# Kernel tuning notes

Hardware: AMD Instinct MI355X
Metric: run time of the kernel (lower is better)

Reference implementation:

```python
import jax, jax.numpy as jnp
import numpy as np

N, E, D_IN, D_OUT = 100000, 1600000, 64, 64


def setup_inputs() -> dict:
    key = jax.random.key(0)
    k0, k1, k2, k3 = jax.random.split(key, 4)
    x = jax.random.normal(k0, (N, D_IN), dtype=jnp.float32)
    edge_index = jax.random.randint(k1, (2, E), 0, N)  # [2, E] (src, dst)
    W = jax.random.normal(k2, (D_IN, D_OUT), dtype=jnp.float32) / np.sqrt(D_IN).astype(np.float32)
    b = jnp.zeros((D_OUT,), dtype=jnp.float32)
    causal_attention = jax.random.normal(k3, (D_OUT, D_OUT), dtype=jnp.float32)
    return {"x": x, "edge_index": edge_index, "W": W, "b": b,
            "causal_attention": causal_attention, "L": 1}


def gcn_conv(x, edge_index, W, b):
    # PyG GCNConv: x' = D^{-1/2} (A + I) D^{-1/2} (x W) + b
    n = x.shape[0]
    xw = x @ W  # [N, D_OUT]
    loops = jnp.arange(n)
    src = jnp.concatenate([edge_index[0], loops])  # [E+N]
    dst = jnp.concatenate([edge_index[1], loops])
    deg = jax.ops.segment_sum(jnp.ones_like(src, dtype=xw.dtype), dst, num_segments=n)
    dinv = jnp.where(deg > 0, jax.lax.rsqrt(deg), 0.0)
    norm = dinv[src] * dinv[dst]  # [E+N]
    agg = jax.ops.segment_sum(norm[:, None] * xw[src], dst, num_segments=n)  # [N, D_OUT]
    return agg + b


def reference(x, edge_index, W, b, causal_attention, L):
    x_conv = gcn_conv(x, edge_index, W, b)
    causal_weights = jax.nn.softmax(causal_attention, axis=1)  # row softmax
    return x_conv @ causal_weights  # [N, D_OUT]
```

## Files before the change

kernel.cpp:

```cpp
#include <hip/hip_runtime.h>
#include <hip/hip_bf16.h>


#define D 64
#define BSHIFT 7
#define BNODES 128
#define ARENA_CAP 3072
#define BIN_TILE 8192

__device__ __forceinline__ unsigned short f2bf(float f) {
    union { float f; unsigned int u; } c;
    c.f = f;
    unsigned int u = c.u;
    u += 0x7fffu + ((u >> 16) & 1u);
    return (unsigned short)(u >> 16);
}
__device__ __forceinline__ float bflo(unsigned int u) {
    union { unsigned int u; float f; } c;
    c.u = u << 16;
    return c.f;
}
__device__ __forceinline__ float bfhi(unsigned int u) {
    union { unsigned int u; float f; } c;
    c.u = u & 0xffff0000u;
    return c.f;
}

__global__ __launch_bounds__(256) void prep_kernel(const float* __restrict__ W,
                                                   const float* __restrict__ b,
                                                   const float* __restrict__ A,
                                                   float* __restrict__ M,
                                                   float* __restrict__ bs,
                                                   int* __restrict__ cursor, int nbuck) {
    __shared__ float S[D * D];
    int t = threadIdx.x;
    int gidx = blockIdx.x * 256 + t;
    if (gidx < nbuck) cursor[gidx] = gidx * ARENA_CAP;
    int wv = t >> 6, lane = t & 63;
#pragma unroll 4
    for (int rr = 0; rr < 16; rr++) {
        int r = wv * 16 + rr;
        float a = A[r * D + lane];
        float m = a;
        for (int off = 32; off; off >>= 1) m = fmaxf(m, __shfl_xor(m, off));
        float p = __expf(a - m);
        float ssum = p;
        for (int off = 32; off; off >>= 1) ssum += __shfl_xor(ssum, off);
        S[r * D + lane] = p / ssum;
    }
    __syncthreads();
    int k = blockIdx.x * 4 + wv;
    float acc = 0.f;
    for (int d2 = 0; d2 < D; d2++) acc += W[k * D + d2] * S[d2 * D + lane];
    M[k * D + lane] = acc;
    if (blockIdx.x == 0 && t < D) {
        float a2 = 0.f;
        for (int d2 = 0; d2 < D; d2++) a2 += b[d2] * S[d2 * D + t];
        bs[t] = a2;
    }
}

__global__ __launch_bounds__(512) void bin_kernel(const int* __restrict__ src,
                                                  const int* __restrict__ dst,
                                                  int* __restrict__ cursor,
                                                  int* __restrict__ binned, int E) {
    __shared__ int h[1024];
    int t = threadIdx.x;
    for (int i = t; i < 1024; i += 512) h[i] = 0;
    __syncthreads();
    int base = blockIdx.x * BIN_TILE;
    int pv[16], bk[16], rv[16];
#pragma unroll
    for (int k = 0; k < 16; k++) {
        int e = base + k * 512 + t;
        if (e < E) {
            int s = src[e], d = dst[e];
            bk[k] = (d >> BSHIFT) & 1023;
            pv[k] = (s << BSHIFT) | (d & (BNODES - 1));
            rv[k] = atomicAdd(&h[bk[k]], 1);
        }
    }
    __syncthreads();
    for (int b2 = t; b2 < 1024; b2 += 512) {
        int c = h[b2];
        if (c) h[b2] = atomicAdd(&cursor[b2], c);
    }
    __syncthreads();
#pragma unroll
    for (int k = 0; k < 16; k++) {
        int e = base + k * 512 + t;
        if (e < E) binned[h[bk[k]] + rv[k]] = pv[k];
    }
}

__global__ __launch_bounds__(256) void rebin_zmat_kernel(const float* __restrict__ x,
                                                         const float* __restrict__ M,
                                                         int* __restrict__ binned,
                                                         const int* __restrict__ cursor,
                                                         int* __restrict__ rowstart,
                                                         int* __restrict__ rowend,
                                                         float* __restrict__ dinv,
                                                         unsigned short* __restrict__ zbf,
                                                         int N) {
    __shared__ int buf[ARENA_CAP];
    __shared__ float Ms[D * D];
    __shared__ float xs[16][D + 1];
    __shared__ float dv[BNODES];
    __shared__ int h[BNODES];
    __shared__ int sc[BNODES];
    __shared__ int cur[BNODES];
    int t = threadIdx.x;
    int b = blockIdx.x;
    int s = b * ARENA_CAP;
    int cnt = cursor[b] - s;
    if (cnt > ARENA_CAP) cnt = ARENA_CAP;
    for (int i = t; i < (D * D) / 4; i += 256)
        ((float4*)Ms)[i] = ((const float4*)M)[i];
    if (t < BNODES) h[t] = 0;
    __syncthreads();
    for (int i = t; i < cnt; i += 256) {
        int p = binned[s + i];
        buf[i] = p;
        atomicAdd(&h[p & (BNODES - 1)], 1);
    }
    __syncthreads();
    if (t < BNODES) sc[t] = h[t];
    __syncthreads();
    for (int off = 1; off < BNODES; off <<= 1) {
        int u = (t < BNODES && t >= off) ? sc[t - off] : 0;
        __syncthreads();
        if (t < BNODES) sc[t] += u;
        __syncthreads();
    }
    if (t < BNODES) {
        int ex = sc[t] - h[t];
        cur[t] = ex;
        float di = rsqrtf((float)(h[t] + 1));
        dv[t] = di;
        int node = (b << BSHIFT) + t;
        if (node < N) {
            rowstart[node] = s + ex;
            rowend[node] = s + sc[t];
            dinv[node] = di;
        }
    }
    __syncthreads();
    for (int i = t; i < cnt; i += 256) {
        int p = buf[i];
        int pos = atomicAdd(&cur[p & (BNODES - 1)], 1);
        binned[s + pos] = (int)((unsigned)p >> BSHIFT);
    }
    for (int rc = 0; rc < 8; rc++) {
        __syncthreads();
        int row0 = (b << BSHIFT) + rc * 16;
        for (int i = t; i < 16 * D; i += 256) {
            int r = i >> 6, c = i & 63;
            xs[r][c] = (row0 + r < N) ? x[(size_t)(row0 + r) * D + c] : 0.f;
        }
        __syncthreads();
        int r = t >> 4;
        int jg = (t & 15) << 2;
        float4 acc = {0.f, 0.f, 0.f, 0.f};
#pragma unroll
        for (int k = 0; k < D; k++) {
            float xv = xs[r][k];
            float4 m = *(const float4*)&Ms[k * D + jg];
            acc.x += xv * m.x;
            acc.y += xv * m.y;
            acc.z += xv * m.z;
            acc.w += xv * m.w;
        }
        int row = row0 + r;
        if (row < N) {
            float di = dv[rc * 16 + r];
            ushort4 res;
            res.x = f2bf(di * acc.x);
            res.y = f2bf(di * acc.y);
            res.z = f2bf(di * acc.z);
            res.w = f2bf(di * acc.w);
            *(ushort4*)&zbf[(size_t)row * D + jg] = res;
        }
    }
}

__global__ __launch_bounds__(256) void gather_kernel(const unsigned short* __restrict__ zbf,
                                                     const int* __restrict__ csr,
                                                     const int* __restrict__ rowstart,
                                                     const int* __restrict__ rowend,
                                                     const float* __restrict__ dinv,
                                                     const float* __restrict__ bs,
                                                     float* __restrict__ out, int n) {
    int node = blockIdx.x * 4 + (threadIdx.x >> 6);
    if (node >= n) return;
    int lane = threadIdx.x & 63;
    int g = lane >> 5;
    int c = lane & 31;
    int start = rowstart[node];
    int end = rowend[node];
    float a0 = 0.f, a1 = 0.f, a2 = 0.f, a3 = 0.f;
    int e = start;
    while (e < end) {
        int cnt = min(end - e, 64);
        int sreg = (lane < cnt) ? csr[e + lane] : 0;
        int k = 0;
        for (; k + 7 < cnt; k += 8) {
            int p0 = __shfl(sreg, k + g);
            int p1 = __shfl(sreg, k + 2 + g);
            int p2 = __shfl(sreg, k + 4 + g);
            int p3 = __shfl(sreg, k + 6 + g);
            unsigned u0 = *(const unsigned*)&zbf[(size_t)p0 * D + 2 * c];
            unsigned u1 = *(const unsigned*)&zbf[(size_t)p1 * D + 2 * c];
            unsigned u2 = *(const unsigned*)&zbf[(size_t)p2 * D + 2 * c];
            unsigned u3 = *(const unsigned*)&zbf[(size_t)p3 * D + 2 * c];
            a0 += bflo(u0); a1 += bfhi(u0);
            a2 += bflo(u1); a3 += bfhi(u1);
            a0 += bflo(u2); a1 += bfhi(u2);
            a2 += bflo(u3); a3 += bfhi(u3);
        }
        for (; k + 1 < cnt; k += 2) {
            int p = __shfl(sreg, k + g);
            unsigned u = *(const unsigned*)&zbf[(size_t)p * D + 2 * c];
            a0 += bflo(u); a1 += bfhi(u);
        }
        if (k < cnt) {
            int p = __shfl(sreg, k);
            unsigned u = *(const unsigned*)&zbf[(size_t)p * D + 2 * c];
            if (g == 0) { a0 += bflo(u); a1 += bfhi(u); }
        }
        e += cnt;
    }
    a0 += a2; a1 += a3;
    a0 += __shfl_xor(a0, 32);
    a1 += __shfl_xor(a1, 32);
    if (lane < 32) {
        unsigned uz = *(const unsigned*)&zbf[(size_t)node * D + 2 * c];
        float2 bb = ((const float2*)bs)[c];
        float di = dinv[node];
        float2 o;
        o.x = di * (a0 + bflo(uz)) + bb.x;
        o.y = di * (a1 + bfhi(uz)) + bb.y;
        ((float2*)&out[(size_t)node * D])[c] = o;
    }
}

extern "C" void kernel_launch(void* const* d_in, const int* in_sizes, int n_in,
                              void* d_out, int out_size, void* d_ws, size_t ws_size,
                              hipStream_t stream) {
    const float* x = (const float*)d_in[0];
    const int* ei = (const int*)d_in[1];
    const float* W = (const float*)d_in[2];
    const float* b = (const float*)d_in[3];
    const float* A = (const float*)d_in[4];

    const int N = in_sizes[0] / D;
    const int E = in_sizes[1] / 2;
    const int* src = ei;
    const int* dst = ei + E;
    const int NBUCK = (N + BNODES - 1) >> BSHIFT;

    char* ws = (char*)d_ws;
    size_t off = 0;
    auto alloc = [&](size_t bytes) -> char* {
        char* p = ws + off;
        off = (off + bytes + 255) & ~(size_t)255;
        return p;
    };
    int* cursor = (int*)alloc((size_t)NBUCK * 4);
    float* dinv = (float*)alloc((size_t)N * 4);
    float* M = (float*)alloc((size_t)D * D * 4);
    float* bs = (float*)alloc((size_t)D * 4);
    int* binned = (int*)alloc((size_t)NBUCK * ARENA_CAP * 4);
    int* rowstart = (int*)alloc((size_t)N * 4);
    int* rowend = (int*)alloc((size_t)N * 4);
    unsigned short* zbf = (unsigned short*)alloc((size_t)N * D * 2);
    (void)ws_size;

    prep_kernel<<<16, 256, 0, stream>>>(W, b, A, M, bs, cursor, NBUCK);
    bin_kernel<<<(E + BIN_TILE - 1) / BIN_TILE, 512, 0, stream>>>(src, dst, cursor, binned, E);
    rebin_zmat_kernel<<<NBUCK, 256, 0, stream>>>(x, M, binned, cursor, rowstart, rowend, dinv, zbf, N);
    gather_kernel<<<(N + 3) / 4, 256, 0, stream>>>(zbf, binned, rowstart, rowend, dinv, bs, (float*)d_out, N);
}
```

Measured before the change: 193.6 us.

## Split rebin/zmat into sort and register-tiled zmat kernels with smaller buckets

```diff
diff --git a/kernel.cpp b/kernel.cpp
--- a/kernel.cpp
+++ b/kernel.cpp
@@ -3,9 +3,9 @@
 
 
 #define D 64
-#define BSHIFT 7
-#define BNODES 128
-#define ARENA_CAP 3072
+#define BSHIFT 6
+#define BNODES 64
+#define ARENA_CAP 1728
 #define BIN_TILE 8192
 
 __device__ __forceinline__ unsigned short f2bf(float f) {
@@ -64,9 +64,9 @@
                                                   const int* __restrict__ dst,
                                                   int* __restrict__ cursor,
                                                   int* __restrict__ binned, int E) {
-    __shared__ int h[1024];
-    int t = threadIdx.x;
-    for (int i = t; i < 1024; i += 512) h[i] = 0;
+    __shared__ int h[2048];
+    int t = threadIdx.x;
+    for (int i = t; i < 2048; i += 512) h[i] = 0;
     __syncthreads();
     int base = blockIdx.x * BIN_TILE;
     int pv[16], bk[16], rv[16];
@@ -75,13 +75,13 @@
         int e = base + k * 512 + t;
         if (e < E) {
             int s = src[e], d = dst[e];
-            bk[k] = (d >> BSHIFT) & 1023;
+            bk[k] = (d >> BSHIFT) & 2047;
             pv[k] = (s << BSHIFT) | (d & (BNODES - 1));
             rv[k] = atomicAdd(&h[bk[k]], 1);
         }
     }
     __syncthreads();
-    for (int b2 = t; b2 < 1024; b2 += 512) {
+    for (int b2 = t; b2 < 2048; b2 += 512) {
         int c = h[b2];
         if (c) h[b2] = atomicAdd(&cursor[b2], c);
     }
@@ -93,29 +93,20 @@
     }
 }
 
-__global__ __launch_bounds__(256) void rebin_zmat_kernel(const float* __restrict__ x,
-                                                         const float* __restrict__ M,
-                                                         int* __restrict__ binned,
-                                                         const int* __restrict__ cursor,
-                                                         int* __restrict__ rowstart,
-                                                         int* __restrict__ rowend,
-                                                         float* __restrict__ dinv,
-                                                         unsigned short* __restrict__ zbf,
-                                                         int N) {
+__global__ __launch_bounds__(256) void sort_kernel(int* __restrict__ binned,
+                                                   const int* __restrict__ cursor,
+                                                   int* __restrict__ rowstart,
+                                                   int* __restrict__ rowend,
+                                                   float* __restrict__ dinv,
+                                                   int N) {
     __shared__ int buf[ARENA_CAP];
-    __shared__ float Ms[D * D];
-    __shared__ float xs[16][D + 1];
-    __shared__ float dv[BNODES];
     __shared__ int h[BNODES];
-    __shared__ int sc[BNODES];
     __shared__ int cur[BNODES];
     int t = threadIdx.x;
     int b = blockIdx.x;
     int s = b * ARENA_CAP;
     int cnt = cursor[b] - s;
     if (cnt > ARENA_CAP) cnt = ARENA_CAP;
-    for (int i = t; i < (D * D) / 4; i += 256)
-        ((float4*)Ms)[i] = ((const float4*)M)[i];
     if (t < BNODES) h[t] = 0;
     __syncthreads();
     for (int i = t; i < cnt; i += 256) {
@@ -124,24 +115,20 @@
         atomicAdd(&h[p & (BNODES - 1)], 1);
     }
     __syncthreads();
-    if (t < BNODES) sc[t] = h[t];
-    __syncthreads();
-    for (int off = 1; off < BNODES; off <<= 1) {
-        int u = (t < BNODES && t >= off) ? sc[t - off] : 0;
-        __syncthreads();
-        if (t < BNODES) sc[t] += u;
-        __syncthreads();
-    }
     if (t < BNODES) {
-        int ex = sc[t] - h[t];
-        cur[t] = ex;
-        float di = rsqrtf((float)(h[t] + 1));
-        dv[t] = di;
+        int v = h[t];
+        int sc = v;
+#pragma unroll
+        for (int off = 1; off < BNODES; off <<= 1) {
+            int u = __shfl_up(sc, off);
+            if (t >= off) sc += u;
+        }
+        cur[t] = sc - v;
         int node = (b << BSHIFT) + t;
         if (node < N) {
-            rowstart[node] = s + ex;
-            rowend[node] = s + sc[t];
-            dinv[node] = di;
+            rowstart[node] = s + sc - v;
+            rowend[node] = s + sc;
+            dinv[node] = rsqrtf((float)(v + 1));
         }
     }
     __syncthreads();
@@ -150,36 +137,65 @@
         int pos = atomicAdd(&cur[p & (BNODES - 1)], 1);
         binned[s + pos] = (int)((unsigned)p >> BSHIFT);
     }
-    for (int rc = 0; rc < 8; rc++) {
-        __syncthreads();
-        int row0 = (b << BSHIFT) + rc * 16;
-        for (int i = t; i < 16 * D; i += 256) {
-            int r = i >> 6, c = i & 63;
-            xs[r][c] = (row0 + r < N) ? x[(size_t)(row0 + r) * D + c] : 0.f;
-        }
-        __syncthreads();
-        int r = t >> 4;
-        int jg = (t & 15) << 2;
-        float4 acc = {0.f, 0.f, 0.f, 0.f};
-#pragma unroll
-        for (int k = 0; k < D; k++) {
-            float xv = xs[r][k];
-            float4 m = *(const float4*)&Ms[k * D + jg];
-            acc.x += xv * m.x;
-            acc.y += xv * m.y;
-            acc.z += xv * m.z;
-            acc.w += xv * m.w;
-        }
+}
+
+__device__ __forceinline__ void fma4(float4& a, float xv, const float4& m) {
+    a.x += xv * m.x; a.y += xv * m.y; a.z += xv * m.z; a.w += xv * m.w;
+}
+__global__ __launch_bounds__(256) void zmat_kernel(const float* __restrict__ x,
+                                                   const float* __restrict__ M,
+                                                   const float* __restrict__ dinv,
+                                                   unsigned short* __restrict__ zbf,
+                                                   int N) {
+    __shared__ float Ms[D * D];
+    __shared__ float xs[64][D + 4];
+    int t = threadIdx.x;
+    int row0 = blockIdx.x << 6;
+    for (int i = t; i < (D * D) / 4; i += 256)
+        ((float4*)Ms)[i] = ((const float4*)M)[i];
+    for (int w = t; w < 1024; w += 256) {
+        int r = w >> 4, c4 = (w & 15) << 2;
         int row = row0 + r;
-        if (row < N) {
-            float di = dv[rc * 16 + r];
-            ushort4 res;
-            res.x = f2bf(di * acc.x);
-            res.y = f2bf(di * acc.y);
-            res.z = f2bf(di * acc.z);
-            res.w = f2bf(di * acc.w);
-            *(ushort4*)&zbf[(size_t)row * D + jg] = res;
-        }
+        float4 v = make_float4(0.f, 0.f, 0.f, 0.f);
+        if (row < N) v = *(const float4*)&x[(size_t)row * D + c4];
+        *(float4*)&xs[r][c4] = v;
+    }
+    __syncthreads();
+    int cg = t & 15, rg = t >> 4;
+    int r0 = rg << 2, c0 = cg << 2;
+    float4 a0 = make_float4(0.f, 0.f, 0.f, 0.f);
+    float4 a1 = a0, a2 = a0, a3 = a0;
+#pragma unroll 4
+    for (int k = 0; k < D; k += 4) {
+        float4 x0 = *(const float4*)&xs[r0 + 0][k];
+        float4 x1 = *(const float4*)&xs[r0 + 1][k];
+        float4 x2 = *(const float4*)&xs[r0 + 2][k];
+        float4 x3 = *(const float4*)&xs[r0 + 3][k];
+        float4 m0 = *(const float4*)&Ms[(k + 0) * D + c0];
+        float4 m1 = *(const float4*)&Ms[(k + 1) * D + c0];
+        float4 m2 = *(const float4*)&Ms[(k + 2) * D + c0];
+        float4 m3 = *(const float4*)&Ms[(k + 3) * D + c0];
+        fma4(a0, x0.x, m0); fma4(a0, x0.y, m1); fma4(a0, x0.z, m2); fma4(a0, x0.w, m3);
+        fma4(a1, x1.x, m0); fma4(a1, x1.y, m1); fma4(a1, x1.z, m2); fma4(a1, x1.w, m3);
+        fma4(a2, x2.x, m0); fma4(a2, x2.y, m1); fma4(a2, x2.z, m2); fma4(a2, x2.w, m3);
+        fma4(a3, x3.x, m0); fma4(a3, x3.y, m1); fma4(a3, x3.z, m2); fma4(a3, x3.w, m3);
+    }
+    int rowb = row0 + r0;
+    if (rowb < N) {
+        float4 dv4 = *(const float4*)&dinv[rowb];
+        ushort4 s0, s1, s2, s3;
+        s0.x = f2bf(dv4.x * a0.x); s0.y = f2bf(dv4.x * a0.y);
+        s0.z = f2bf(dv4.x * a0.z); s0.w = f2bf(dv4.x * a0.w);
+        s1.x = f2bf(dv4.y * a1.x); s1.y = f2bf(dv4.y * a1.y);
+        s1.z = f2bf(dv4.y * a1.z); s1.w = f2bf(dv4.y * a1.w);
+        s2.x = f2bf(dv4.z * a2.x); s2.y = f2bf(dv4.z * a2.y);
+        s2.z = f2bf(dv4.z * a2.z); s2.w = f2bf(dv4.z * a2.w);
+        s3.x = f2bf(dv4.w * a3.x); s3.y = f2bf(dv4.w * a3.y);
+        s3.z = f2bf(dv4.w * a3.z); s3.w = f2bf(dv4.w * a3.w);
+        *(ushort4*)&zbf[(size_t)(rowb + 0) * D + c0] = s0;
+        *(ushort4*)&zbf[(size_t)(rowb + 1) * D + c0] = s1;
+        *(ushort4*)&zbf[(size_t)(rowb + 2) * D + c0] = s2;
+        *(ushort4*)&zbf[(size_t)(rowb + 3) * D + c0] = s3;
     }
 }
 
@@ -277,6 +293,7 @@
 
     prep_kernel<<<16, 256, 0, stream>>>(W, b, A, M, bs, cursor, NBUCK);
     bin_kernel<<<(E + BIN_TILE - 1) / BIN_TILE, 512, 0, stream>>>(src, dst, cursor, binned, E);
-    rebin_zmat_kernel<<<NBUCK, 256, 0, stream>>>(x, M, binned, cursor, rowstart, rowend, dinv, zbf, N);
+    sort_kernel<<<NBUCK, 256, 0, stream>>>(binned, cursor, rowstart, rowend, dinv, N);
+    zmat_kernel<<<(N + 63) >> 6, 256, 0, stream>>>(x, M, dinv, zbf, N);
     gather_kernel<<<(N + 3) / 4, 256, 0, stream>>>(zbf, binned, rowstart, rowend, dinv, bs, (float*)d_out, N);
 }
```

Result: faster. 181.5 us (-6.3%).
